# Optimization experiments

Hardware: AMD Instinct MI355X
Metric: run time of the kernel (lower is better)

The kernel has to match this reference:

```python
import jax, jax.numpy as jnp
import numpy as np

N_EMBD = 768
HEAD_SIZE = 64

def setup_inputs() -> dict:
    key = jax.random.key(0)
    ks = jax.random.split(key, 9)
    B, S = 8, 2048
    scale = 1.0 / np.sqrt(N_EMBD)
    return {
        "q": jax.random.normal(ks[0], (B, S, N_EMBD), jnp.float32),
        "k": jax.random.normal(ks[1], (B, S, N_EMBD), jnp.float32),
        "v": jax.random.normal(ks[2], (B, S, N_EMBD), jnp.float32),
        "Wq": jax.random.normal(ks[3], (N_EMBD, HEAD_SIZE), jnp.float32) * scale,
        "bq": jnp.zeros((HEAD_SIZE,), jnp.float32),
        "Wk": jax.random.normal(ks[4], (N_EMBD, HEAD_SIZE), jnp.float32) * scale,
        "bk": jnp.zeros((HEAD_SIZE,), jnp.float32),
        "Wv": jax.random.normal(ks[5], (N_EMBD, HEAD_SIZE), jnp.float32) * scale,
        "bv": jnp.zeros((HEAD_SIZE,), jnp.float32),
    }

def reference(q, k, v, Wq, bq, Wk, bk, Wv, bv):
    # NOTE: original scales by sqrt(C) where C = n_embd (input dim), not head_size.
    C = q.shape[-1]
    qi = q @ Wq + bq  # [B,S,H]
    ki = k @ Wk + bk
    vi = v @ Wv + bv
    att = jnp.einsum('bsh,bth->bst', qi, ki) / jnp.sqrt(jnp.float32(C))
    att = jax.nn.softmax(att, axis=-1)
    out = jnp.einsum('bst,bth->bsh', att, vi)
    return out
```

## Files before the change

### kernel.cpp

```cpp
#include <hip/hip_runtime.h>

#define Bn 8
#define Sn 2048
#define Cn 768
#define Hn 64
#define BS (Bn * Sn)

typedef __attribute__((ext_vector_type(8))) short bf16x8;
typedef __attribute__((ext_vector_type(4))) float f32x4;

__device__ __forceinline__ unsigned short f2bf(float x) {
  unsigned int u = __builtin_bit_cast(unsigned int, x);
  u += 0x7FFFu + ((u >> 16) & 1u);
  return (unsigned short)(u >> 16);
}

__device__ __forceinline__ void gload_lds16(const void* g, void* l) {
  __builtin_amdgcn_global_load_lds(
      (const __attribute__((address_space(1))) unsigned int*)g,
      (__attribute__((address_space(3))) unsigned int*)l, 16, 0, 0);
}

__global__ __launch_bounds__(256) void wconv(const float* __restrict__ Wq,
                                             const float* __restrict__ Wk,
                                             const float* __restrict__ Wv,
                                             unsigned short* __restrict__ Wt) {
  int idx = blockIdx.x * 256 + threadIdx.x;
  int mat = idx / (Cn * Hn);
  int rem = idx - mat * (Cn * Hn);
  int c = rem / Hn, h = rem - c * Hn;
  const float* W = (mat == 0) ? Wq : (mat == 1) ? Wk : Wv;
  Wt[mat * (Hn * Cn) + h * Cn + c] = f2bf(W[rem]);
}

__global__ __launch_bounds__(256) void proj(const float* __restrict__ q,
                                            const float* __restrict__ k,
                                            const float* __restrict__ v,
                                            const float* __restrict__ bq,
                                            const float* __restrict__ bk,
                                            const float* __restrict__ bv,
                                            const unsigned short* __restrict__ Wt,
                                            unsigned short* __restrict__ qi,
                                            unsigned short* __restrict__ ki,
                                            unsigned short* __restrict__ vi) {
  const int mat  = blockIdx.x >> 8;
  const int row0 = (blockIdx.x & 255) * 64;
  const float* X    = (mat == 0) ? q  : (mat == 1) ? k  : v;
  const float* bias = (mat == 0) ? bq : (mat == 1) ? bk : bv;
  unsigned short* Y = (mat == 0) ? qi : (mat == 1) ? ki : vi;
  const unsigned short* Wm = Wt + mat * (Hn * Cn);
  const float scale = (mat == 0) ? 0.03608439182435161f : 1.0f;

  __shared__ __align__(16) float          Xf[2][4096];
  __shared__ __align__(16) unsigned short Wl[2][4096];

  const int tid  = threadIdx.x;
  const int lane = tid & 63;
  const int w    = tid >> 6;
  const int col  = lane & 15;
  const int grp  = lane >> 4;

  const float* xsrc[4];
#pragma unroll
  for (int j = 0; j < 4; ++j) {
    int sidx = j * 256 + tid;
    int row  = sidx >> 4;
    int cf4  = (sidx & 15) ^ (row & 15);
    xsrc[j]  = X + (size_t)(row0 + row) * Cn + cf4 * 4;
  }
  const unsigned short* wsrc[2];
#pragma unroll
  for (int j = 0; j < 2; ++j) {
    int sidx = j * 256 + tid;
    int h    = sidx >> 3;
    int pd   = (sidx & 7) ^ (h & 7);
    wsrc[j]  = Wm + (size_t)h * Cn + pd * 8;
  }

#pragma unroll
  for (int j = 0; j < 4; ++j) gload_lds16(xsrc[j], &Xf[0][(j * 256 + w * 64) * 4]);
#pragma unroll
  for (int j = 0; j < 2; ++j) gload_lds16(wsrc[j], &Wl[0][(j * 256 + w * 64) * 8]);
#pragma unroll
  for (int j = 0; j < 4; ++j) gload_lds16(xsrc[j] + 64, &Xf[1][(j * 256 + w * 64) * 4]);
#pragma unroll
  for (int j = 0; j < 2; ++j) gload_lds16(wsrc[j] + 64, &Wl[1][(j * 256 + w * 64) * 8]);

  f32x4 acc[4] = {};
  const int rloc = w * 16 + col;

#pragma unroll
  for (int c = 0; c < 12; ++c) {
    const int buf = c & 1;
    if (c == 11) {
      asm volatile("s_waitcnt vmcnt(0)" ::: "memory");
    } else {
      asm volatile("s_waitcnt vmcnt(6)" ::: "memory");
    }
    __builtin_amdgcn_s_barrier();
    __builtin_amdgcn_sched_barrier(0);
#pragma unroll
    for (int ks = 0; ks < 2; ++ks) {
      const int cf0 = ks * 8 + grp * 2;
      float4 a0 = *(const float4*)&Xf[buf][(rloc * 16 + (cf0 ^ col)) * 4];
      float4 a1 = *(const float4*)&Xf[buf][(rloc * 16 + ((cf0 + 1) ^ col)) * 4];
      bf16x8 av;
      av[0] = (short)f2bf(a0.x); av[1] = (short)f2bf(a0.y);
      av[2] = (short)f2bf(a0.z); av[3] = (short)f2bf(a0.w);
      av[4] = (short)f2bf(a1.x); av[5] = (short)f2bf(a1.y);
      av[6] = (short)f2bf(a1.z); av[7] = (short)f2bf(a1.w);
      const int p = ks * 4 + grp;
#pragma unroll
      for (int nf = 0; nf < 4; ++nf) {
        int h = nf * 16 + col;
        bf16x8 bfr = *(const bf16x8*)&Wl[buf][(h * 8 + (p ^ (h & 7))) * 8];
        acc[nf] = __builtin_amdgcn_mfma_f32_16x16x32_bf16(av, bfr, acc[nf], 0, 0, 0);
      }
    }
    __builtin_amdgcn_sched_barrier(0);
    __builtin_amdgcn_s_barrier();
    __builtin_amdgcn_sched_barrier(0);
    if (c < 10) {
#pragma unroll
      for (int j = 0; j < 4; ++j)
        gload_lds16(xsrc[j] + (c + 2) * 64, &Xf[buf][(j * 256 + w * 64) * 4]);
#pragma unroll
      for (int j = 0; j < 2; ++j)
        gload_lds16(wsrc[j] + (c + 2) * 64, &Wl[buf][(j * 256 + w * 64) * 8]);
    }
  }

#pragma unroll
  for (int nf = 0; nf < 4; ++nf) {
    int h = nf * 16 + col;
    float bb = bias[h];
#pragma unroll
    for (int r2 = 0; r2 < 4; ++r2) {
      int row = row0 + w * 16 + grp * 4 + r2;
      Y[(size_t)row * Hn + h] = f2bf((acc[nf][r2] + bb) * scale);
    }
  }
}

template <int SPLIT>
__global__ __launch_bounds__(256) void attn(const unsigned short* __restrict__ qi,
                                            const unsigned short* __restrict__ ki,
                                            const unsigned short* __restrict__ vi,
                                            float* __restrict__ pacc,
                                            float* __restrict__ pm,
                                            float* __restrict__ pl,
                                            float* __restrict__ out,
                                            int tpb) {
  const int bq    = blockIdx.x & 255;
  const int split = blockIdx.x >> 8;
  const int b  = bq >> 5;
  const int s0 = (bq & 31) * 64;
  const int t0 = split * tpb;
  const unsigned short* Qb = qi + ((size_t)b * Sn + s0) * Hn;
  const unsigned short* Kb = ki + (size_t)b * Sn * Hn;
  const unsigned short* Vb = vi + (size_t)b * Sn * Hn;

  __shared__ __align__(16) unsigned char Ks[64 * 128];
  __shared__ __align__(16) unsigned char Vt[64 * 128];
  __shared__ __align__(16) unsigned char Ps[4 * 16 * 128];

  const int tid  = threadIdx.x;
  const int lane = tid & 63;
  const int w    = tid >> 6;
  const int col  = lane & 15;
  const int grp  = lane >> 4;

  bf16x8 qa[2];
#pragma unroll
  for (int ks2 = 0; ks2 < 2; ++ks2)
    qa[ks2] = *(const bf16x8*)(Qb + (size_t)(w * 16 + col) * Hn + ks2 * 32 + grp * 8);

  f32x4 acc[4] = {};
  float m[4], l[4];
#pragma unroll
  for (int r = 0; r < 4; ++r) { m[r] = -1e30f; l[r] = 0.0f; }

  for (int t = t0; t < t0 + tpb; ++t) {
    const unsigned short* Kt = Kb + t * 64 * Hn;
    const unsigned short* Vg = Vb + t * 64 * Hn;
    __syncthreads();
    {
      int kr = tid >> 2, p = tid & 3;
      const uint4* src = (const uint4*)(Kt + kr * Hn);
      uint4 a  = src[p * 2];
      uint4 b2 = src[p * 2 + 1];
      *(uint4*)(Ks + kr * 128 + ((p * 32) ^ ((kr & 7) << 4)))        = a;
      *(uint4*)(Ks + kr * 128 + (((p * 32) + 16) ^ ((kr & 7) << 4))) = b2;
    }
    {
      int kp = tid >> 3;
      int dg = tid & 7;
      uint4 v0 = *(const uint4*)(Vg + (2 * kp) * Hn + dg * 8);
      uint4 v1 = *(const uint4*)(Vg + (2 * kp + 1) * Hn + dg * 8);
      const unsigned short* a0 = (const unsigned short*)&v0;
      const unsigned short* a1 = (const unsigned short*)&v1;
#pragma unroll
      for (int j0 = 0; j0 < 8; ++j0) {
        int j = (j0 + dg) & 7;
        int d = dg * 8 + j;
        unsigned int pk = (unsigned int)a0[j] | ((unsigned int)a1[j] << 16);
        *(unsigned int*)(Vt + d * 128 + ((4 * kp) ^ ((d & 7) << 4))) = pk;
      }
    }
    __syncthreads();
    f32x4 sf[4] = {};
#pragma unroll
    for (int ks2 = 0; ks2 < 2; ++ks2) {
#pragma unroll
      for (int nf = 0; nf < 4; ++nf) {
        int kr = nf * 16 + col;
        bf16x8 bfr = *(const bf16x8*)(Ks + kr * 128 + ((ks2 * 64 + grp * 16) ^ ((kr & 7) << 4)));
        sf[nf] = __builtin_amdgcn_mfma_f32_16x16x32_bf16(qa[ks2], bfr, sf[nf], 0, 0, 0);
      }
    }
    float mn[4], fs[4];
#pragma unroll
    for (int r = 0; r < 4; ++r) {
      float mx = fmaxf(fmaxf(sf[0][r], sf[1][r]), fmaxf(sf[2][r], sf[3][r]));
#pragma unroll
      for (int off = 1; off < 16; off <<= 1)
        mx = fmaxf(mx, __shfl_xor(mx, off, 64));
      mn[r] = fmaxf(m[r], mx);
      fs[r] = __expf(m[r] - mn[r]);
      m[r]  = mn[r];
    }
#pragma unroll
    for (int nf = 0; nf < 4; ++nf)
#pragma unroll
      for (int r = 0; r < 4; ++r)
        sf[nf][r] = __expf(sf[nf][r] - mn[r]);
#pragma unroll
    for (int r = 0; r < 4; ++r) {
      float sm = sf[0][r] + sf[1][r] + sf[2][r] + sf[3][r];
#pragma unroll
      for (int off = 1; off < 16; off <<= 1)
        sm += __shfl_xor(sm, off, 64);
      l[r] = l[r] * fs[r] + sm;
    }
#pragma unroll
    for (int nf = 0; nf < 4; ++nf) {
#pragma unroll
      for (int r = 0; r < 4; ++r) {
        acc[nf][r] *= fs[r];
        int prow = grp * 4 + r;
        int key  = nf * 16 + col;
        *(unsigned short*)(Ps + w * 2048 + prow * 128 + ((key * 2) ^ ((prow & 7) << 4))) =
            f2bf(sf[nf][r]);
      }
    }
#pragma unroll
    for (int kk = 0; kk < 2; ++kk) {
      bf16x8 pa = *(const bf16x8*)(Ps + w * 2048 + col * 128 +
                                   ((kk * 64 + grp * 16) ^ ((col & 7) << 4)));
#pragma unroll
      for (int nf = 0; nf < 4; ++nf) {
        int dr = nf * 16 + col;
        bf16x8 bv = *(const bf16x8*)(Vt + dr * 128 + ((kk * 64 + grp * 16) ^ ((dr & 7) << 4)));
        acc[nf] = __builtin_amdgcn_mfma_f32_16x16x32_bf16(pa, bv, acc[nf], 0, 0, 0);
      }
    }
  }
  if (SPLIT) {
    const size_t sb = (size_t)split * BS + (size_t)b * Sn;
#pragma unroll
    for (int nf = 0; nf < 4; ++nf) {
#pragma unroll
      for (int r = 0; r < 4; ++r) {
        int row = s0 + w * 16 + grp * 4 + r;
        pacc[(sb + row) * Hn + nf * 16 + col] = acc[nf][r];
      }
    }
    if (col == 0) {
#pragma unroll
      for (int r = 0; r < 4; ++r) {
        int row = s0 + w * 16 + grp * 4 + r;
        pm[sb + row] = m[r];
        pl[sb + row] = l[r];
      }
    }
  } else {
#pragma unroll
    for (int nf = 0; nf < 4; ++nf) {
#pragma unroll
      for (int r = 0; r < 4; ++r) {
        int row = s0 + w * 16 + grp * 4 + r;
        out[((size_t)b * Sn + row) * Hn + nf * 16 + col] = acc[nf][r] / l[r];
      }
    }
  }
}

__global__ __launch_bounds__(256) void combine(const float* __restrict__ pacc,
                                               const float* __restrict__ pm,
                                               const float* __restrict__ pl,
                                               float* __restrict__ out,
                                               int nsplit) {
  int gid = blockIdx.x * 256 + threadIdx.x;
  int gr  = gid >> 4;
  int dq  = (gid & 15) * 4;
  float M = -1e30f;
  for (int s = 0; s < nsplit; ++s) M = fmaxf(M, pm[(size_t)s * BS + gr]);
  float L = 0.0f;
  float4 o = make_float4(0.f, 0.f, 0.f, 0.f);
  for (int s = 0; s < nsplit; ++s) {
    float wgt = __expf(pm[(size_t)s * BS + gr] - M);
    L += pl[(size_t)s * BS + gr] * wgt;
    float4 p = *(const float4*)(pacc + ((size_t)s * BS + gr) * Hn + dq);
    o.x += p.x * wgt; o.y += p.y * wgt; o.z += p.z * wgt; o.w += p.w * wgt;
  }
  float inv = 1.0f / L;
  float4 r = make_float4(o.x * inv, o.y * inv, o.z * inv, o.w * inv);
  *(float4*)(out + (size_t)gr * Hn + dq) = r;
}

extern "C" void kernel_launch(void* const* d_in, const int* in_sizes, int n_in,
                              void* d_out, int out_size, void* d_ws, size_t ws_size,
                              hipStream_t stream) {
  const float* q  = (const float*)d_in[0];
  const float* k  = (const float*)d_in[1];
  const float* v  = (const float*)d_in[2];
  const float* Wq = (const float*)d_in[3];
  const float* bq = (const float*)d_in[4];
  const float* Wk = (const float*)d_in[5];
  const float* bk = (const float*)d_in[6];
  const float* Wv = (const float*)d_in[7];
  const float* bv = (const float*)d_in[8];
  float* out = (float*)d_out;

  unsigned short* Wt = (unsigned short*)d_ws;
  unsigned short* qi = Wt + 3 * Hn * Cn;
  unsigned short* ki = qi + (size_t)BS * Hn;
  unsigned short* vi = ki + (size_t)BS * Hn;
  float* pacc = (float*)(vi + (size_t)BS * Hn);

  const size_t base_bytes = (size_t)(3 * Hn * Cn + 3 * (size_t)BS * Hn) * 2;
  const size_t avail = (ws_size > base_bytes) ? ws_size - base_bytes : 0;

  int nsplit = 4;
  while (nsplit > 1 &&
         (size_t)nsplit * ((size_t)BS * Hn * 4 + 2 * (size_t)BS * 4) > avail)
    nsplit >>= 1;
  bool direct = ((size_t)nsplit * ((size_t)BS * Hn * 4 + 2 * (size_t)BS * 4) > avail);

  float* pm = pacc + (size_t)nsplit * BS * Hn;
  float* pl = pm + (size_t)nsplit * BS;

  wconv<<<dim3((3 * Cn * Hn) / 256), dim3(256), 0, stream>>>(Wq, Wk, Wv, Wt);
  proj<<<dim3(768), dim3(256), 0, stream>>>(q, k, v, bq, bk, bv, Wt, qi, ki, vi);
  if (direct) {
    attn<0><<<dim3(256), dim3(256), 0, stream>>>(qi, ki, vi, nullptr, nullptr, nullptr, out, 32);
  } else {
    attn<1><<<dim3(256 * nsplit), dim3(256), 0, stream>>>(qi, ki, vi, pacc, pm, pl, nullptr,
                                                          32 / nsplit);
    combine<<<dim3(BS * 16 / 256), dim3(256), 0, stream>>>(pacc, pm, pl, out, nsplit);
  }
}
```

Measured before the change: 87.31 us.

## Pre-convert activations to bf16 and use async LDS-loaded projection kernel

Adds a separate pass that converts q, k and v from fp32 to bf16 into workspace scratch, then a new projection kernel that streams those bf16 rows into LDS with direct global-to-LDS loads, double buffering and a swizzled layout feeding MFMA. The intent is to make the projection GEMM's input staging cheaper and better pipelined. The cost is an extra full read of the fp32 inputs plus a write and re-read of bf16 copies, and more kernel launches. The scratch region is reused for the split-attention partials, and the path is only taken when the workspace is large enough.

```diff
diff --git a/kernel.cpp b/kernel.cpp
--- a/kernel.cpp
+++ b/kernel.cpp
@@ -31,6 +31,119 @@
   int c = rem / Hn, h = rem - c * Hn;
   const float* W = (mat == 0) ? Wq : (mat == 1) ? Wk : Wv;
   Wt[mat * (Hn * Cn) + h * Cn + c] = f2bf(W[rem]);
+}
+
+__global__ __launch_bounds__(256) void xconv(const float* __restrict__ src,
+                                             unsigned short* __restrict__ dst, int n4) {
+  int stride = gridDim.x * 256;
+  for (int i = blockIdx.x * 256 + threadIdx.x; i < n4; i += stride) {
+    float4 xv = *(const float4*)(src + (size_t)i * 4);
+    ushort4 hv;
+    hv.x = f2bf(xv.x); hv.y = f2bf(xv.y); hv.z = f2bf(xv.z); hv.w = f2bf(xv.w);
+    *(ushort4*)(dst + (size_t)i * 4) = hv;
+  }
+}
+
+__global__ __launch_bounds__(256) void projb(const unsigned short* __restrict__ qx,
+                                             const unsigned short* __restrict__ kx,
+                                             const unsigned short* __restrict__ vx,
+                                             const float* __restrict__ bq,
+                                             const float* __restrict__ bk,
+                                             const float* __restrict__ bv,
+                                             const unsigned short* __restrict__ Wt,
+                                             unsigned short* __restrict__ qi,
+                                             unsigned short* __restrict__ ki,
+                                             unsigned short* __restrict__ vi) {
+  const int mat  = blockIdx.x >> 8;
+  const int row0 = (blockIdx.x & 255) * 64;
+  const unsigned short* X = (mat == 0) ? qx : (mat == 1) ? kx : vx;
+  const float* bias = (mat == 0) ? bq : (mat == 1) ? bk : bv;
+  unsigned short* Y = (mat == 0) ? qi : (mat == 1) ? ki : vi;
+  const unsigned short* Wm = Wt + mat * (Hn * Cn);
+  const float scale = (mat == 0) ? 0.03608439182435161f : 1.0f;
+
+  __shared__ __align__(16) unsigned short Xl[2][4096];
+  __shared__ __align__(16) unsigned short Wl[2][4096];
+
+  const int tid  = threadIdx.x;
+  const int lane = tid & 63;
+  const int w    = tid >> 6;
+  const int col  = lane & 15;
+  const int grp  = lane >> 4;
+
+  const unsigned short* xsrc[2];
+#pragma unroll
+  for (int j = 0; j < 2; ++j) {
+    int sidx = j * 256 + tid;
+    int xr   = sidx >> 3;
+    int xs   = (sidx & 7) ^ (xr & 7);
+    xsrc[j]  = X + (size_t)(row0 + xr) * Cn + xs * 8;
+  }
+  const unsigned short* wsrc[2];
+#pragma unroll
+  for (int j = 0; j < 2; ++j) {
+    int sidx = j * 256 + tid;
+    int h    = sidx >> 3;
+    int pd   = (sidx & 7) ^ (h & 7);
+    wsrc[j]  = Wm + (size_t)h * Cn + pd * 8;
+  }
+
+#pragma unroll
+  for (int j = 0; j < 2; ++j) gload_lds16(xsrc[j], &Xl[0][(j * 256 + w * 64) * 8]);
+#pragma unroll
+  for (int j = 0; j < 2; ++j) gload_lds16(wsrc[j], &Wl[0][(j * 256 + w * 64) * 8]);
+#pragma unroll
+  for (int j = 0; j < 2; ++j) gload_lds16(xsrc[j] + 64, &Xl[1][(j * 256 + w * 64) * 8]);
+#pragma unroll
+  for (int j = 0; j < 2; ++j) gload_lds16(wsrc[j] + 64, &Wl[1][(j * 256 + w * 64) * 8]);
+
+  f32x4 acc[4] = {};
+  const int rloc = w * 16 + col;
+
+#pragma unroll
+  for (int c = 0; c < 12; ++c) {
+    const int buf = c & 1;
+    if (c == 11) {
+      asm volatile("s_waitcnt vmcnt(0)" ::: "memory");
+    } else {
+      asm volatile("s_waitcnt vmcnt(4)" ::: "memory");
+    }
+    __builtin_amdgcn_s_barrier();
+    __builtin_amdgcn_sched_barrier(0);
+#pragma unroll
+    for (int ks = 0; ks < 2; ++ks) {
+      const int s = ks * 4 + grp;
+      bf16x8 av = *(const bf16x8*)&Xl[buf][(rloc * 8 + (s ^ (rloc & 7))) * 8];
+#pragma unroll
+      for (int nf = 0; nf < 4; ++nf) {
+        int h = nf * 16 + col;
+        bf16x8 bfr = *(const bf16x8*)&Wl[buf][(h * 8 + (s ^ (h & 7))) * 8];
+        acc[nf] = __builtin_amdgcn_mfma_f32_16x16x32_bf16(av, bfr, acc[nf], 0, 0, 0);
+      }
+    }
+    __builtin_amdgcn_sched_barrier(0);
+    __builtin_amdgcn_s_barrier();
+    __builtin_amdgcn_sched_barrier(0);
+    if (c < 10) {
+#pragma unroll
+      for (int j = 0; j < 2; ++j)
+        gload_lds16(xsrc[j] + (c + 2) * 64, &Xl[buf][(j * 256 + w * 64) * 8]);
+#pragma unroll
+      for (int j = 0; j < 2; ++j)
+        gload_lds16(wsrc[j] + (c + 2) * 64, &Wl[buf][(j * 256 + w * 64) * 8]);
+    }
+  }
+
+#pragma unroll
+  for (int nf = 0; nf < 4; ++nf) {
+    int h = nf * 16 + col;
+    float bb = bias[h];
+#pragma unroll
+    for (int r2 = 0; r2 < 4; ++r2) {
+      int row = row0 + w * 16 + grp * 4 + r2;
+      Y[(size_t)row * Hn + h] = f2bf((acc[nf][r2] + bb) * scale);
+    }
+  }
 }
 
 __global__ __launch_bounds__(256) void proj(const float* __restrict__ q,
@@ -336,10 +449,14 @@
   unsigned short* qi = Wt + 3 * Hn * Cn;
   unsigned short* ki = qi + (size_t)BS * Hn;
   unsigned short* vi = ki + (size_t)BS * Hn;
-  float* pacc = (float*)(vi + (size_t)BS * Hn);
+  unsigned short* scratch = vi + (size_t)BS * Hn;
 
   const size_t base_bytes = (size_t)(3 * Hn * Cn + 3 * (size_t)BS * Hn) * 2;
   const size_t avail = (ws_size > base_bytes) ? ws_size - base_bytes : 0;
+
+  const size_t xe = (size_t)BS * Cn;
+  const size_t xconv_bytes = 3 * xe * 2;
+  bool use_xc = (avail >= xconv_bytes);
 
   int nsplit = 4;
   while (nsplit > 1 &&
@@ -347,11 +464,23 @@
     nsplit >>= 1;
   bool direct = ((size_t)nsplit * ((size_t)BS * Hn * 4 + 2 * (size_t)BS * 4) > avail);
 
-  float* pm = pacc + (size_t)nsplit * BS * Hn;
-  float* pl = pm + (size_t)nsplit * BS;
+  unsigned short* qx = scratch;
+  unsigned short* kx = qx + xe;
+  unsigned short* vx = kx + xe;
+  float* pacc = (float*)scratch;
+  float* pm   = pacc + (size_t)nsplit * BS * Hn;
+  float* pl   = pm + (size_t)nsplit * BS;
 
   wconv<<<dim3((3 * Cn * Hn) / 256), dim3(256), 0, stream>>>(Wq, Wk, Wv, Wt);
-  proj<<<dim3(768), dim3(256), 0, stream>>>(q, k, v, bq, bk, bv, Wt, qi, ki, vi);
+  if (use_xc) {
+    const int n4 = (int)(xe / 4);
+    xconv<<<dim3(2048), dim3(256), 0, stream>>>(q, qx, n4);
+    xconv<<<dim3(2048), dim3(256), 0, stream>>>(k, kx, n4);
+    xconv<<<dim3(2048), dim3(256), 0, stream>>>(v, vx, n4);
+    projb<<<dim3(768), dim3(256), 0, stream>>>(qx, kx, vx, bq, bk, bv, Wt, qi, ki, vi);
+  } else {
+    proj<<<dim3(768), dim3(256), 0, stream>>>(q, k, v, bq, bk, bv, Wt, qi, ki, vi);
+  }
   if (direct) {
     attn<0><<<dim3(256), dim3(256), 0, stream>>>(qi, ki, vi, nullptr, nullptr, nullptr, out, 32);
   } else {
```

Result: slower. 112.6 us (+29.0%).
